# Optimization experiments

Hardware: AMD Instinct MI355X
Metric: run time of the kernel (lower is better)

The kernel has to match this reference:

```python
import jax, jax.numpy as jnp
import numpy as np

E = 8
D_IN = 1024
D_HID = 4096
D_OUT = 1024
N_TOK = 32768  # total tokens; equal split of 4096 per expert


def setup_inputs() -> dict:
    key = jax.random.key(0)
    k_in, k_w1, k_w2 = jax.random.split(key, 3)
    inputs = jax.random.normal(k_in, (N_TOK, D_IN), dtype=jnp.float32)
    expert_size = jnp.full((E,), N_TOK // E, dtype=jnp.int64)
    # reset_parameters: normal(0, 1/sqrt(fan_in)) per expert
    w1 = jax.random.normal(k_w1, (E, D_IN, D_HID), dtype=jnp.float32) / np.sqrt(D_IN)
    b1 = jnp.zeros((E, D_HID), dtype=jnp.float32)
    w2 = jax.random.normal(k_w2, (E, D_HID, D_OUT), dtype=jnp.float32) / np.sqrt(D_HID)
    b2 = jnp.zeros((E, D_OUT), dtype=jnp.float32)
    return {"inputs": inputs, "expert_size": expert_size,
            "w1": w1, "b1": b1, "w2": w2, "b2": b2}


def reference(inputs, expert_size, w1, b1, w2, b2):
    # Grouped GEMM over contiguous per-expert splits. expert_size is equal
    # per expert (N_TOK // E), so the variable-split loop in the torch code
    # collapses to a batched einsum with identical math.
    e = w1.shape[0]
    n, d = inputs.shape
    cap = n // e  # tokens per expert (equal splits)
    x = inputs.reshape(e, cap, d)                       # [E, cap, D_IN]
    h = jnp.einsum('ecd,edh->ech', x, w1) + b1[:, None, :]
    h = jax.nn.gelu(h, approximate=False)               # F.gelu default = erf gelu
    y = jnp.einsum('ech,eho->eco', h, w2) + b2[:, None, :]
    return y.reshape(n, -1)                             # [N_TOK, D_OUT]
```

## Files before the change

kernel.cpp:

```cpp
#include <hip/hip_runtime.h>
#include <hip/hip_bf16.h>

#define NE 8
#define DIN 1024
#define DHID 4096
#define DOUTD 1024
#define NTOK 32768
#define CAP (NTOK / NE)

typedef unsigned short u16;
typedef __attribute__((ext_vector_type(8))) short bf16x8;
typedef __attribute__((ext_vector_type(4))) float f32x4;

__device__ __forceinline__ u16 f2bf(float x) {
  unsigned u = __builtin_bit_cast(unsigned, x);
  u += 0x7fffu + ((u >> 16) & 1u);
  return (u16)(u >> 16);
}

__device__ __forceinline__ float gelu_erf(float x) {
  return 0.5f * x * (1.0f + erff(x * 0.70710678118654752f));
}

__device__ __forceinline__ void async_ld16(const void* g, void* l) {
  __builtin_amdgcn_global_load_lds(
      (const __attribute__((address_space(1))) unsigned int*)g,
      (__attribute__((address_space(3))) unsigned int*)l, 16, 0, 0);
}

__global__ __launch_bounds__(256) void convert_bf16_kernel(const float* __restrict__ in,
                                                           u16* __restrict__ out) {
  size_t i = ((size_t)blockIdx.x * 256 + threadIdx.x) * 8;
  float4 a = *(const float4*)(in + i);
  float4 b = *(const float4*)(in + i + 4);
  uint4 o;
  o.x = (unsigned)f2bf(a.x) | ((unsigned)f2bf(a.y) << 16);
  o.y = (unsigned)f2bf(a.z) | ((unsigned)f2bf(a.w) << 16);
  o.z = (unsigned)f2bf(b.x) | ((unsigned)f2bf(b.y) << 16);
  o.w = (unsigned)f2bf(b.z) | ((unsigned)f2bf(b.w) << 16);
  *(uint4*)(out + i) = o;
}

__global__ __launch_bounds__(256) void transpose_bf16_kernel(const float* __restrict__ in,
                                                             u16* __restrict__ out,
                                                             int K, int N) {
  __shared__ __align__(16) u16 tile[64 * 72];
  const int e = blockIdx.z;
  const int n0 = blockIdx.x * 64;
  const int k0 = blockIdx.y * 64;
  const float* inp = in + (size_t)e * K * N;
  u16* outp = out + (size_t)e * N * K;
  const int t = threadIdx.x;
  const int kr = t >> 4;
  const int nc = (t & 15) * 4;
#pragma unroll
  for (int rr = 0; rr < 4; ++rr) {
    int kl = rr * 16 + kr;
    float4 v = *(const float4*)(inp + (size_t)(k0 + kl) * N + n0 + nc);
    tile[(nc + 0) * 72 + kl] = f2bf(v.x);
    tile[(nc + 1) * 72 + kl] = f2bf(v.y);
    tile[(nc + 2) * 72 + kl] = f2bf(v.z);
    tile[(nc + 3) * 72 + kl] = f2bf(v.w);
  }
  __syncthreads();
  const int nr = t >> 3;
  const int kc = (t & 7) * 8;
#pragma unroll
  for (int it = 0; it < 2; ++it) {
    int nl = it * 32 + nr;
    bf16x8 w = *(const bf16x8*)(tile + nl * 72 + kc);
    *(bf16x8*)(outp + (size_t)(n0 + nl) * K + k0 + kc) = w;
  }
}

template <int K, int N, bool GELU_OUT>
__global__ __launch_bounds__(256) void moe_gemm_kernel(const u16* __restrict__ A,
                                                       const u16* __restrict__ Bt,
                                                       const float* __restrict__ bias,
                                                       void* __restrict__ Out) {
  __shared__ __align__(16) u16 lds_a[128 * 64];
  __shared__ __align__(16) u16 lds_b[128 * 64];
  const int e = blockIdx.z;
  const int m0 = blockIdx.y * 128;
  const int n0 = blockIdx.x * 128;
  const u16* Ae = A + (size_t)e * CAP * K;
  const u16* Be = Bt + (size_t)e * N * K;

  const int t = threadIdx.x;
  const int lane = t & 63;
  const int wv = t >> 6;
  const int wm = (wv >> 1) * 64;
  const int wn = (wv & 1) * 64;

  f32x4 acc[4][4] = {};

  const int sr = wv * 8 + (lane >> 3);
  const int su = lane & 7;
  const int g  = lane >> 4;
  const int rl = lane & 15;

  for (int kt = 0; kt < K / 64; ++kt) {
    if (kt) __syncthreads();
    const int kb = kt * 64;
#pragma unroll
    for (int it = 0; it < 4; ++it) {
      int r = it * 32 + sr;
      int uo = su ^ (r & 7);
      async_ld16(Ae + (size_t)(m0 + r) * K + kb + uo * 8,
                 lds_a + (it * 32 + wv * 8) * 64);
    }
#pragma unroll
    for (int it = 0; it < 4; ++it) {
      int r = it * 32 + sr;
      int uo = su ^ (r & 7);
      async_ld16(Be + (size_t)(n0 + r) * K + kb + uo * 8,
                 lds_b + (it * 32 + wv * 8) * 64);
    }
    __syncthreads();
#pragma unroll
    for (int kk = 0; kk < 64; kk += 32) {
      const int uu = (kk >> 3) + g;
      bf16x8 bfr[4], afr[4];
#pragma unroll
      for (int i = 0; i < 4; ++i) {
        int row = wn + i * 16 + rl;
        bfr[i] = *(const bf16x8*)(lds_b + row * 64 + ((uu ^ (row & 7)) << 3));
      }
#pragma unroll
      for (int j = 0; j < 4; ++j) {
        int row = wm + j * 16 + rl;
        afr[j] = *(const bf16x8*)(lds_a + row * 64 + ((uu ^ (row & 7)) << 3));
      }
#pragma unroll
      for (int i = 0; i < 4; ++i)
#pragma unroll
        for (int j = 0; j < 4; ++j)
          acc[i][j] = __builtin_amdgcn_mfma_f32_16x16x32_bf16(bfr[i], afr[j],
                                                              acc[i][j], 0, 0, 0);
    }
  }

  const float* be = bias + (size_t)e * N;
  const int mb = m0 + wm + rl;
  const int nb = n0 + wn + g * 4;
  if constexpr (GELU_OUT) {
    u16* Oe = (u16*)Out + (size_t)e * CAP * N;
#pragma unroll
    for (int j = 0; j < 4; ++j) {
      int m = mb + j * 16;
#pragma unroll
      for (int i = 0; i < 4; ++i) {
        int n = nb + i * 16;
        float4 bv = *(const float4*)(be + n);
        ushort4 o;
        o.x = f2bf(gelu_erf(acc[i][j][0] + bv.x));
        o.y = f2bf(gelu_erf(acc[i][j][1] + bv.y));
        o.z = f2bf(gelu_erf(acc[i][j][2] + bv.z));
        o.w = f2bf(gelu_erf(acc[i][j][3] + bv.w));
        *(ushort4*)(Oe + (size_t)m * N + n) = o;
      }
    }
  } else {
    float* Oe = (float*)Out + (size_t)e * CAP * N;
#pragma unroll
    for (int j = 0; j < 4; ++j) {
      int m = mb + j * 16;
#pragma unroll
      for (int i = 0; i < 4; ++i) {
        int n = nb + i * 16;
        float4 bv = *(const float4*)(be + n);
        float4 o;
        o.x = acc[i][j][0] + bv.x;
        o.y = acc[i][j][1] + bv.y;
        o.z = acc[i][j][2] + bv.z;
        o.w = acc[i][j][3] + bv.w;
        *(float4*)(Oe + (size_t)m * N + n) = o;
      }
    }
  }
}

extern "C" void kernel_launch(void* const* d_in, const int* in_sizes, int n_in,
                              void* d_out, int out_size, void* d_ws, size_t ws_size,
                              hipStream_t stream) {
  const float* x  = (const float*)d_in[0];
  const float* w1 = (const float*)d_in[2];
  const float* b1 = (const float*)d_in[3];
  const float* w2 = (const float*)d_in[4];
  const float* b2 = (const float*)d_in[5];
  float* out = (float*)d_out;

  char* wsp = (char*)d_ws;
  u16* x_bf = (u16*)(wsp);
  u16* w1t  = (u16*)(wsp + (size_t)67108864);
  u16* w2t  = (u16*)(wsp + (size_t)134217728);
  u16* h    = (u16*)(wsp + (size_t)201326592);

  convert_bf16_kernel<<<(NTOK * DIN) / (256 * 8), 256, 0, stream>>>(x, x_bf);
  transpose_bf16_kernel<<<dim3(DHID / 64, DIN / 64, NE), 256, 0, stream>>>(w1, w1t, DIN, DHID);
  transpose_bf16_kernel<<<dim3(DOUTD / 64, DHID / 64, NE), 256, 0, stream>>>(w2, w2t, DHID, DOUTD);

  moe_gemm_kernel<DIN, DHID, true>
      <<<dim3(DHID / 128, CAP / 128, NE), 256, 0, stream>>>(x_bf, w1t, b1, h);
  moe_gemm_kernel<DHID, DOUTD, false>
      <<<dim3(DOUTD / 128, CAP / 128, NE), 256, 0, stream>>>(h, w2t, b2, out);
}
```

Measured before the change: 836.4 us.

## Rewrite grouped GEMM with 256x256 tiles and 4-stage async LDS pipeline

Replaces the 128x128, 256-thread GEMM with 256x256 tiles, 512 threads and a 4-deep ring of LDS buffers (128 KB dynamic shared memory) filled by async global-to-LDS loads, so loads for later k-steps overlap the MFMAs of the current one. It uses explicit vmcnt waits and barriers, raises MFMA priority with s_setprio, and interleaves experts in a flat 1D grid. The larger tiles raise arithmetic intensity, at the cost of more registers per thread (32 accumulators) and heavy LDS use, which limits occupancy.

Measured after the change: 781.9 us. -6.5%, faster.

```diff
diff --git a/kernel.cpp b/kernel.cpp
--- a/kernel.cpp
+++ b/kernel.cpp
@@ -1,5 +1,6 @@
 #include <hip/hip_runtime.h>
 #include <hip/hip_bf16.h>
+#include <type_traits>
 
 #define NE 8
 #define DIN 1024
@@ -74,106 +75,137 @@
 }
 
 template <int K, int N, bool GELU_OUT>
-__global__ __launch_bounds__(256) void moe_gemm_kernel(const u16* __restrict__ A,
-                                                       const u16* __restrict__ Bt,
-                                                       const float* __restrict__ bias,
-                                                       void* __restrict__ Out) {
-  __shared__ __align__(16) u16 lds_a[128 * 64];
-  __shared__ __align__(16) u16 lds_b[128 * 64];
-  const int e = blockIdx.z;
-  const int m0 = blockIdx.y * 128;
-  const int n0 = blockIdx.x * 128;
+__global__ __launch_bounds__(512, 2) void moe_gemm256_kernel(
+    const u16* __restrict__ A, const u16* __restrict__ Bt,
+    const float* __restrict__ bias, void* __restrict__ Out) {
+  extern __shared__ __align__(16) char smem[];
+  constexpr int TX = N / 256;
+  constexpr int NT = K / 32;
+
+  const int bid = blockIdx.x;
+  const int e = bid & 7;
+  const int idx = bid >> 3;
+  const int ty = idx / TX;
+  const int tx = idx % TX;
+  const int m0 = ty * 256;
+  const int n0 = tx * 256;
+
   const u16* Ae = A + (size_t)e * CAP * K;
   const u16* Be = Bt + (size_t)e * N * K;
 
   const int t = threadIdx.x;
-  const int lane = t & 63;
-  const int wv = t >> 6;
-  const int wm = (wv >> 1) * 64;
-  const int wn = (wv & 1) * 64;
-
-  f32x4 acc[4][4] = {};
-
-  const int sr = wv * 8 + (lane >> 3);
-  const int su = lane & 7;
-  const int g  = lane >> 4;
-  const int rl = lane & 15;
-
-  for (int kt = 0; kt < K / 64; ++kt) {
-    if (kt) __syncthreads();
-    const int kb = kt * 64;
-#pragma unroll
-    for (int it = 0; it < 4; ++it) {
-      int r = it * 32 + sr;
-      int uo = su ^ (r & 7);
-      async_ld16(Ae + (size_t)(m0 + r) * K + kb + uo * 8,
-                 lds_a + (it * 32 + wv * 8) * 64);
+  const int l = t & 63;
+  const int w = t >> 6;
+  const int wr = w >> 2;
+  const int wc = w & 3;
+  const int g = l >> 4;
+  const int rl = l & 15;
+
+  const int ul = (l & 7) ^ (l >> 3);
+  const int skk = (ul & 3) * 8;
+  const int srhi = (ul >> 2) << 7;
+  size_t sa[2], sb[2];
+  int chunkbase[2];
+#pragma unroll
+  for (int it = 0; it < 2; ++it) {
+    int chunk = it * 8 + w;
+    int rowp = chunk * 8 + (l >> 3);
+    sa[it] = (size_t)(m0 + rowp + srhi) * K + skk;
+    sb[it] = (size_t)(n0 + rowp + srhi) * K + skk;
+    chunkbase[it] = chunk * 1024;
+  }
+
+  int aoff[8], boff[4];
+#pragma unroll
+  for (int j = 0; j < 8; ++j) {
+    int rp = j * 16 + rl;
+    aoff[j] = rp * 128 + (((wr * 4 + g) ^ (rl & 7)) << 4);
+  }
+#pragma unroll
+  for (int i = 0; i < 4; ++i) {
+    int rp = (wc & 1) * 64 + i * 16 + rl;
+    boff[i] = 16384 + rp * 128 + ((((wc >> 1) * 4 + g) ^ (rl & 7)) << 4);
+  }
+
+  f32x4 acc[8][4] = {};
+
+  auto stage = [&](int tt) {
+    char* dst = smem + (size_t)(tt & 3) * 32768;
+    const size_t kb = (size_t)tt * 32;
+#pragma unroll
+    for (int it = 0; it < 2; ++it)
+      async_ld16(Ae + sa[it] + kb, dst + chunkbase[it]);
+#pragma unroll
+    for (int it = 0; it < 2; ++it)
+      async_ld16(Be + sb[it] + kb, dst + 16384 + chunkbase[it]);
+  };
+
+  stage(0);
+  stage(1);
+  stage(2);
+  asm volatile("s_waitcnt vmcnt(8)\n\ts_barrier" ::: "memory");
+
+  auto kiter = [&](int tt, auto STG, auto WN) {
+    if constexpr (decltype(STG)::value) stage(tt + 3);
+    const char* src = smem + (size_t)(tt & 3) * 32768;
+    bf16x8 afr[8], bfr[4];
+#pragma unroll
+    for (int i = 0; i < 4; ++i) bfr[i] = *(const bf16x8*)(src + boff[i]);
+#pragma unroll
+    for (int j = 0; j < 8; ++j) afr[j] = *(const bf16x8*)(src + aoff[j]);
+    __builtin_amdgcn_s_setprio(1);
+#pragma unroll
+    for (int j = 0; j < 8; ++j)
+#pragma unroll
+      for (int i = 0; i < 4; ++i)
+        acc[j][i] = __builtin_amdgcn_mfma_f32_16x16x32_bf16(bfr[i], afr[j], acc[j][i], 0, 0, 0);
+    __builtin_amdgcn_s_setprio(0);
+    constexpr int WNv = decltype(WN)::value;
+    if constexpr (WNv >= 0) {
+      asm volatile("s_waitcnt vmcnt(%0)\n\ts_barrier" :: "n"(WNv) : "memory");
     }
-#pragma unroll
-    for (int it = 0; it < 4; ++it) {
-      int r = it * 32 + sr;
-      int uo = su ^ (r & 7);
-      async_ld16(Be + (size_t)(n0 + r) * K + kb + uo * 8,
-                 lds_b + (it * 32 + wv * 8) * 64);
-    }
-    __syncthreads();
-#pragma unroll
-    for (int kk = 0; kk < 64; kk += 32) {
-      const int uu = (kk >> 3) + g;
-      bf16x8 bfr[4], afr[4];
-#pragma unroll
-      for (int i = 0; i < 4; ++i) {
-        int row = wn + i * 16 + rl;
-        bfr[i] = *(const bf16x8*)(lds_b + row * 64 + ((uu ^ (row & 7)) << 3));
-      }
-#pragma unroll
-      for (int j = 0; j < 4; ++j) {
-        int row = wm + j * 16 + rl;
-        afr[j] = *(const bf16x8*)(lds_a + row * 64 + ((uu ^ (row & 7)) << 3));
-      }
-#pragma unroll
-      for (int i = 0; i < 4; ++i)
-#pragma unroll
-        for (int j = 0; j < 4; ++j)
-          acc[i][j] = __builtin_amdgcn_mfma_f32_16x16x32_bf16(bfr[i], afr[j],
-                                                              acc[i][j], 0, 0, 0);
-    }
-  }
+  };
+
+  for (int tt = 0; tt < NT - 3; ++tt)
+    kiter(tt, std::true_type{}, std::integral_constant<int, 8>{});
+  kiter(NT - 3, std::false_type{}, std::integral_constant<int, 4>{});
+  kiter(NT - 2, std::false_type{}, std::integral_constant<int, 0>{});
+  kiter(NT - 1, std::false_type{}, std::integral_constant<int, -1>{});
 
   const float* be = bias + (size_t)e * N;
-  const int mb = m0 + wm + rl;
-  const int nb = n0 + wn + g * 4;
+  const int mb = m0 + wr * 128 + rl;
+  const int nb = n0 + wc * 64 + g * 4;
   if constexpr (GELU_OUT) {
-    u16* Oe = (u16*)Out + (size_t)e * CAP * N;
-#pragma unroll
-    for (int j = 0; j < 4; ++j) {
+    u16* Oe = (u16*)Out + (size_t)e * (size_t)CAP * N;
+#pragma unroll
+    for (int j = 0; j < 8; ++j) {
       int m = mb + j * 16;
 #pragma unroll
       for (int i = 0; i < 4; ++i) {
         int n = nb + i * 16;
         float4 bv = *(const float4*)(be + n);
         ushort4 o;
-        o.x = f2bf(gelu_erf(acc[i][j][0] + bv.x));
-        o.y = f2bf(gelu_erf(acc[i][j][1] + bv.y));
-        o.z = f2bf(gelu_erf(acc[i][j][2] + bv.z));
-        o.w = f2bf(gelu_erf(acc[i][j][3] + bv.w));
+        o.x = f2bf(gelu_erf(acc[j][i][0] + bv.x));
+        o.y = f2bf(gelu_erf(acc[j][i][1] + bv.y));
+        o.z = f2bf(gelu_erf(acc[j][i][2] + bv.z));
+        o.w = f2bf(gelu_erf(acc[j][i][3] + bv.w));
         *(ushort4*)(Oe + (size_t)m * N + n) = o;
       }
     }
   } else {
-    float* Oe = (float*)Out + (size_t)e * CAP * N;
-#pragma unroll
-    for (int j = 0; j < 4; ++j) {
+    float* Oe = (float*)Out + (size_t)e * (size_t)CAP * N;
+#pragma unroll
+    for (int j = 0; j < 8; ++j) {
       int m = mb + j * 16;
 #pragma unroll
       for (int i = 0; i < 4; ++i) {
         int n = nb + i * 16;
         float4 bv = *(const float4*)(be + n);
         float4 o;
-        o.x = acc[i][j][0] + bv.x;
-        o.y = acc[i][j][1] + bv.y;
-        o.z = acc[i][j][2] + bv.z;
-        o.w = acc[i][j][3] + bv.w;
+        o.x = acc[j][i][0] + bv.x;
+        o.y = acc[j][i][1] + bv.y;
+        o.z = acc[j][i][2] + bv.z;
+        o.w = acc[j][i][3] + bv.w;
         *(float4*)(Oe + (size_t)m * N + n) = o;
       }
     }
@@ -196,12 +228,17 @@
   u16* w2t  = (u16*)(wsp + (size_t)134217728);
   u16* h    = (u16*)(wsp + (size_t)201326592);
 
+  hipFuncSetAttribute(reinterpret_cast<const void*>(moe_gemm256_kernel<DIN, DHID, true>),
+                      hipFuncAttributeMaxDynamicSharedMemorySize, 131072);
+  hipFuncSetAttribute(reinterpret_cast<const void*>(moe_gemm256_kernel<DHID, DOUTD, false>),
+                      hipFuncAttributeMaxDynamicSharedMemorySize, 131072);
+
   convert_bf16_kernel<<<(NTOK * DIN) / (256 * 8), 256, 0, stream>>>(x, x_bf);
   transpose_bf16_kernel<<<dim3(DHID / 64, DIN / 64, NE), 256, 0, stream>>>(w1, w1t, DIN, DHID);
   transpose_bf16_kernel<<<dim3(DOUTD / 64, DHID / 64, NE), 256, 0, stream>>>(w2, w2t, DHID, DOUTD);
 
-  moe_gemm_kernel<DIN, DHID, true>
-      <<<dim3(DHID / 128, CAP / 128, NE), 256, 0, stream>>>(x_bf, w1t, b1, h);
-  moe_gemm_kernel<DHID, DOUTD, false>
-      <<<dim3(DOUTD / 128, CAP / 128, NE), 256, 0, stream>>>(h, w2t, b2, out);
-}
+  moe_gemm256_kernel<DIN, DHID, true>
+      <<<dim3(NE * (CAP / 256) * (DHID / 256)), 512, 131072, stream>>>(x_bf, w1t, b1, h);
+  moe_gemm256_kernel<DHID, DOUTD, false>
+      <<<dim3(NE * (CAP / 256) * (DOUTD / 256)), 512, 131072, stream>>>(h, w2t, b2, out);
+}
```
